# Kernel tuning notes

Hardware: AMD Instinct MI355X
Metric: run time of the kernel (lower is better)

## Reference

```python
import jax, jax.numpy as jnp
import numpy as np

D_MODEL = 1024
NUM_HEADS = 16
D_K = D_MODEL // NUM_HEADS
B, L = 2, 4096


def setup_inputs() -> dict:
    key = jax.random.key(0)
    ks = jax.random.split(key, 12)
    s = 0.02
    return {
        "q": jax.random.normal(ks[0], (B, L, D_MODEL), dtype=jnp.float32),
        "k": jax.random.normal(ks[1], (B, L, D_MODEL), dtype=jnp.float32),
        "v": jax.random.normal(ks[2], (B, L, D_MODEL), dtype=jnp.float32),
        "Wq": jax.random.normal(ks[3], (D_MODEL, D_MODEL), dtype=jnp.float32) * s,
        "bq": jax.random.normal(ks[4], (D_MODEL,), dtype=jnp.float32) * s,
        "Wk": jax.random.normal(ks[5], (D_MODEL, D_MODEL), dtype=jnp.float32) * s,
        "bk": jax.random.normal(ks[6], (D_MODEL,), dtype=jnp.float32) * s,
        "Wv": jax.random.normal(ks[7], (D_MODEL, D_MODEL), dtype=jnp.float32) * s,
        "bv": jax.random.normal(ks[8], (D_MODEL,), dtype=jnp.float32) * s,
        "Wo": jax.random.normal(ks[9], (D_MODEL, D_MODEL), dtype=jnp.float32) * s,
        "bo": jax.random.normal(ks[10], (D_MODEL,), dtype=jnp.float32) * s,
    }


def reference(q, k, v, Wq, bq, Wk, bk, Wv, bv, Wo, bo):
    b, l, _ = q.shape
    # projections (torch Linear: x @ W.T + b), reshape to [b, l, h, d]
    qf = (q @ Wq.T + bq).reshape(b, l, NUM_HEADS, D_K)
    kf = (k @ Wk.T + bk).reshape(b, l, NUM_HEADS, D_K)
    vf = (v @ Wv.T + bv).reshape(b, l, NUM_HEADS, D_K)
    # elu+1 feature map (positive features)
    qf = jax.nn.elu(qf) + 1.0
    kf = jax.nn.elu(kf) + 1.0
    # normalizer uses full-sequence k sum (as in the original code)
    z = 1.0 / (jnp.einsum("blhd,bhd->blh", qf, kf.sum(axis=1)) + 1e-6)
    # cumulative sums over sequence (the linear-attention scan state)
    k_cum = jnp.cumsum(kf, axis=1)  # [b, l, h, d]
    v_cum = jnp.cumsum(vf, axis=1)  # [b, l, h, d]
    context = jnp.einsum("blhd,blhd->blh", qf, k_cum)  # [b, l, h]
    context = context[..., None] * v_cum * z[..., None]  # [b, l, h, d]
    context = context.reshape(b, l, NUM_HEADS * D_K)
    return context @ Wo.T + bo
```

## Files before the change

kernel.cpp:

```cpp
#include <hip/hip_runtime.h>
#include <hip/hip_bf16.h>
#include <cstdint>
#include <cstddef>

#define D_MODEL 1024
#define NUM_HEADS 16
#define DK_DIM 64
#define BATCH 2
#define SEQ 4096
#define MROWS (BATCH*SEQ)
#define NCHUNK 128
#define CHUNK 32

#define BM 128
#define BN 128
#define BK 64
#define KTILES (D_MODEL/BK)

typedef __attribute__((ext_vector_type(4))) float f32x4;
typedef __attribute__((ext_vector_type(2))) float f32x2;
typedef __attribute__((ext_vector_type(8))) short bf16x8;
typedef __attribute__((ext_vector_type(4))) short s16x4;
typedef __attribute__((ext_vector_type(2))) uint32_t u32x2;
typedef __attribute__((ext_vector_type(4))) uint32_t u32x4;

__device__ __forceinline__ float b2f(short s) {
  union { uint32_t u; float f; } c; c.u = ((uint32_t)(uint16_t)s) << 16; return c.f;
}
__device__ __forceinline__ short f2b(float f) {
  union { float f; uint32_t u; } c; c.f = f;
  uint32_t u = c.u;
  u += 0x7FFFu + ((u >> 16) & 1u);
  return (short)(u >> 16);
}
__device__ __forceinline__ f32x4 b4_to_f4(s16x4 s) {
  f32x4 r;
  r.x = b2f(s.x); r.y = b2f(s.y); r.z = b2f(s.z); r.w = b2f(s.w);
  return r;
}
__device__ __forceinline__ uint32_t cvtpk(float lo, float hi) {
  uint32_t r;
  asm("v_cvt_pk_bf16_f32 %0, %1, %2" : "=v"(r) : "v"(lo), "v"(hi));
  return r;
}

__global__ __launch_bounds__(256) void cvt_w4(
    const float* __restrict__ s0, const float* __restrict__ s1,
    const float* __restrict__ s2, const float* __restrict__ s3,
    short* __restrict__ dst) {
  const int y = blockIdx.y;
  const float* s = (y == 0) ? s0 : (y == 1) ? s1 : (y == 2) ? s2 : s3;
  const int i = blockIdx.x * 256 + threadIdx.x;
  float4 v = reinterpret_cast<const float4*>(s)[i];
  s16x4 o;
  o.x = f2b(v.x); o.y = f2b(v.y); o.z = f2b(v.z); o.w = f2b(v.w);
  reinterpret_cast<s16x4*>(dst)[(size_t)y * (D_MODEL * D_MODEL / 4) + i] = o;
}

template<int AFP32, int OUTBF16>
__global__ __launch_bounds__(256, 3) void gemm4(
    const void* __restrict__ A0, const void* __restrict__ A1,
    const void* __restrict__ A2, const short* __restrict__ Wbase,
    const float* __restrict__ b0, const float* __restrict__ b1,
    const float* __restrict__ b2, void* __restrict__ Cbase, int actmask)
{
  __shared__ short lds[(BM + BN) * BK];
  const int tid = threadIdx.x;
  const int wid = tid >> 6;
  const int lane = tid & 63;
  const int brow = blockIdx.x * BM;
  const int bcol = blockIdx.y * BN;
  const int z = blockIdx.z;
  const int wr = wid >> 1, wc = wid & 1;

  const void* Ap = (z == 0) ? A0 : (z == 1) ? A1 : A2;
  const float* bias = (z == 0) ? b0 : (z == 1) ? b1 : b2;
  const short* Bw = Wbase + (size_t)z * D_MODEL * D_MODEL;
  const int act = (actmask >> z) & 1;
  const float* __restrict__ A32 = (const float*)Ap;
  const short* __restrict__ A16 = (const short*)Ap;

  f32x4 acc[4][4];
#pragma unroll
  for (int i = 0; i < 4; ++i)
#pragma unroll
    for (int j = 0; j < 4; ++j)
#pragma unroll
      for (int t = 0; t < 4; ++t) acc[i][j][t] = 0.f;

  const int srow = lane >> 3;
  const int gql  = lane & 7;

  float4 abuf32[8];
  u32x4  abuf16[4];

  auto loadA = [&](int t) {
    const int k0 = t * BK;
#pragma unroll
    for (int i = 0; i < 4; ++i) {
      const int row = brow + i * 32 + wid * 8 + srow;
      if constexpr (AFP32) {
        const float* src = A32 + (size_t)row * D_MODEL + k0 + gql * 8;
        abuf32[2 * i]     = *reinterpret_cast<const float4*>(src);
        abuf32[2 * i + 1] = *reinterpret_cast<const float4*>(src + 4);
      } else {
        abuf16[i] = *reinterpret_cast<const u32x4*>(A16 + (size_t)row * D_MODEL + k0 + gql * 8);
      }
    }
  };
  auto writeA = [&]() {
#pragma unroll
    for (int i = 0; i < 4; ++i) {
      u32x4 w;
      if constexpr (AFP32) {
        w.x = cvtpk(abuf32[2 * i].x,     abuf32[2 * i].y);
        w.y = cvtpk(abuf32[2 * i].z,     abuf32[2 * i].w);
        w.z = cvtpk(abuf32[2 * i + 1].x, abuf32[2 * i + 1].y);
        w.w = cvtpk(abuf32[2 * i + 1].z, abuf32[2 * i + 1].w);
      } else {
        w = abuf16[i];
      }
      const int ebyte = (i * 32 + wid * 8 + srow) * 128 + gql * 16;
      *reinterpret_cast<u32x4*>((char*)lds + ebyte) = w;
    }
  };
  auto stageB = [&](int t) {
    short* sB = lds + BM * BK;
    const int k0 = t * BK;
#pragma unroll
    for (int i = 0; i < 4; ++i) {
      const int r = i * 32 + wid * 8;
      const short* g = Bw + (size_t)(bcol + r + srow) * D_MODEL + k0 + gql * 8;
      __builtin_amdgcn_global_load_lds((const __attribute__((address_space(1))) void*)g,
          (__attribute__((address_space(3))) void*)(sB + r * BK), 16, 0, 0);
    }
  };

  const int lane15 = lane & 15;
  const int kq = (lane >> 4) * 16;

  auto compute = [&]() {
    const char* sAb = (const char*)lds;
    const char* sBb = sAb + BM * BK * 2;
#pragma unroll
    for (int ks = 0; ks < 2; ++ks) {
      bf16x8 Af[4], Bf[4];
#pragma unroll
      for (int mi = 0; mi < 4; ++mi)
        Af[mi] = *reinterpret_cast<const bf16x8*>(
            sAb + (wr * 64 + mi * 16 + lane15) * 128 + ks * 64 + kq);
#pragma unroll
      for (int nj = 0; nj < 4; ++nj)
        Bf[nj] = *reinterpret_cast<const bf16x8*>(
            sBb + (wc * 64 + nj * 16 + lane15) * 128 + ks * 64 + kq);
#pragma unroll
      for (int mi = 0; mi < 4; ++mi)
#pragma unroll
        for (int nj = 0; nj < 4; ++nj)
          acc[mi][nj] = __builtin_amdgcn_mfma_f32_16x16x32_bf16(Bf[nj], Af[mi], acc[mi][nj], 0, 0, 0);
    }
  };

  loadA(0);
#pragma unroll 1
  for (int t = 0; t < KTILES; ++t) {
    asm volatile("s_waitcnt lgkmcnt(0)" ::: "memory");
    __builtin_amdgcn_s_barrier();
    stageB(t);
    asm volatile("s_waitcnt vmcnt(4)" ::: "memory");
    writeA();
    if (t + 1 < KTILES) loadA(t + 1);
    asm volatile("s_waitcnt lgkmcnt(0)" ::: "memory");
    if (t + 1 < KTILES) {
      if constexpr (AFP32) asm volatile("s_waitcnt vmcnt(8)" ::: "memory");
      else                 asm volatile("s_waitcnt vmcnt(4)" ::: "memory");
    } else {
      asm volatile("s_waitcnt vmcnt(0)" ::: "memory");
    }
    __builtin_amdgcn_s_barrier();
    __builtin_amdgcn_sched_barrier(0);
    compute();
  }

  const int csub4 = (lane >> 4) * 4;
#pragma unroll
  for (int mi = 0; mi < 4; ++mi) {
    const int row = brow + wr * 64 + mi * 16 + lane15;
    const size_t rowbase = (size_t)z * MROWS * D_MODEL + (size_t)row * D_MODEL;
#pragma unroll
    for (int nj = 0; nj < 4; ++nj) {
      const int col0 = bcol + wc * 64 + nj * 16 + csub4;
      const float4 bv = *reinterpret_cast<const float4*>(&bias[col0]);
      float v0 = acc[mi][nj][0] + bv.x;
      float v1 = acc[mi][nj][1] + bv.y;
      float v2 = acc[mi][nj][2] + bv.z;
      float v3 = acc[mi][nj][3] + bv.w;
      if (act) {
        v0 = (v0 > 0.f) ? (v0 + 1.f) : __expf(v0);
        v1 = (v1 > 0.f) ? (v1 + 1.f) : __expf(v1);
        v2 = (v2 > 0.f) ? (v2 + 1.f) : __expf(v2);
        v3 = (v3 > 0.f) ? (v3 + 1.f) : __expf(v3);
      }
      if (OUTBF16) {
        u32x2 w;
        w.x = cvtpk(v0, v1);
        w.y = cvtpk(v2, v3);
        *reinterpret_cast<u32x2*>(&((short*)Cbase)[rowbase + col0]) = w;
      } else {
        float4 w; w.x = v0; w.y = v1; w.z = v2; w.w = v3;
        *reinterpret_cast<float4*>(&((float*)Cbase)[rowbase + col0]) = w;
      }
    }
  }
}

__global__ __launch_bounds__(256) void chunk_sums(
    const short* __restrict__ kf, const short* __restrict__ vf,
    float* __restrict__ ck, float* __restrict__ cv)
{
  const int gw = blockIdx.x * 4 + (threadIdx.x >> 6);
  const int lane = threadIdx.x & 63;
  const int c = gw & (NCHUNK - 1);
  const int h = (gw >> 7) & (NUM_HEADS - 1);
  const int b = gw >> 11;
  const int half = lane >> 5;
  const int dpair = (lane & 31) * 2;
  const size_t base = ((size_t)(b * SEQ + c * CHUNK) * NUM_HEADS + h) * DK_DIM + dpair;

  float skx = 0.f, sky = 0.f, svx = 0.f, svy = 0.f;
#pragma unroll
  for (int i = 0; i < CHUNK / 2; ++i) {
    const size_t off = base + (size_t)(2 * i + half) * D_MODEL;
    uint32_t ku = *reinterpret_cast<const uint32_t*>(&kf[off]);
    uint32_t vu = *reinterpret_cast<const uint32_t*>(&vf[off]);
    skx += b2f((short)(ku & 0xffff)); sky += b2f((short)(ku >> 16));
    svx += b2f((short)(vu & 0xffff)); svy += b2f((short)(vu >> 16));
  }
  skx += __shfl_xor(skx, 32, 64); sky += __shfl_xor(sky, 32, 64);
  svx += __shfl_xor(svx, 32, 64); svy += __shfl_xor(svy, 32, 64);
  if (half == 0) {
    const size_t o = ((size_t)((b * NUM_HEADS + h) * NCHUNK + c)) * DK_DIM + dpair;
    f32x2 a; a.x = skx; a.y = sky;
    f32x2 bb; bb.x = svx; bb.y = svy;
    *reinterpret_cast<f32x2*>(&ck[o]) = a;
    *reinterpret_cast<f32x2*>(&cv[o]) = bb;
  }
}

__global__ __launch_bounds__(64) void chunk_scan(
    float* __restrict__ ck, float* __restrict__ cv, float* __restrict__ ksum)
{
  const int bh = blockIdx.x;
  const int d = threadIdx.x;
  float rk = 0.f, rv = 0.f;
#pragma unroll 8
  for (int c = 0; c < NCHUNK; ++c) {
    const size_t o = ((size_t)(bh * NCHUNK + c)) * DK_DIM + d;
    const float tk = ck[o], tv = cv[o];
    ck[o] = rk; cv[o] = rv;
    rk += tk; rv += tv;
  }
  ksum[bh * DK_DIM + d] = rk;
}

__global__ __launch_bounds__(256) void scan_ctx(
    const short* __restrict__ qf, const short* __restrict__ kf,
    const short* __restrict__ vf,
    const float* __restrict__ ck, const float* __restrict__ cv,
    const float* __restrict__ ksum, short* __restrict__ ctx)
{
  const int gw = blockIdx.x * 4 + (threadIdx.x >> 6);
  const int lane = threadIdx.x & 63;
  const int pg = lane >> 4;
  const int dg = lane & 15;
  const int c = gw & (NCHUNK - 1);
  const int h = (gw >> 7) & (NUM_HEADS - 1);
  const int b = gw >> 11;
  const int bh = b * NUM_HEADS + h;
  const int d4 = dg * 4;

  f32x4 krun = *reinterpret_cast<const f32x4*>(
      &ck[((size_t)(bh * NCHUNK + c)) * DK_DIM + d4]);
  f32x4 vrun = *reinterpret_cast<const f32x4*>(
      &cv[((size_t)(bh * NCHUNK + c)) * DK_DIM + d4]);
  const f32x4 kst = *reinterpret_cast<const f32x4*>(&ksum[bh * DK_DIM + d4]);

  const size_t base = ((size_t)(b * SEQ + c * CHUNK) * NUM_HEADS + h) * DK_DIM + d4;

  for (int p0 = 0; p0 < CHUNK; p0 += 4) {
    const size_t qoff = base + (size_t)(p0 + pg) * D_MODEL;
    const f32x4 q4 = b4_to_f4(*reinterpret_cast<const s16x4*>(&qf[qoff]));
    f32x4 sk, sv;
#pragma unroll
    for (int i = 0; i < 4; ++i) {
      const size_t off = base + (size_t)(p0 + i) * D_MODEL;
      krun += b4_to_f4(*reinterpret_cast<const s16x4*>(&kf[off]));
      vrun += b4_to_f4(*reinterpret_cast<const s16x4*>(&vf[off]));
      if (i == pg) { sk = krun; sv = vrun; }
    }
    float s1 = q4.x * sk.x + q4.y * sk.y + q4.z * sk.z + q4.w * sk.w;
    float s2 = q4.x * kst.x + q4.y * kst.y + q4.z * kst.z + q4.w * kst.w;
#pragma unroll
    for (int m = 1; m < 16; m <<= 1) {
      s1 += __shfl_xor(s1, m, 64);
      s2 += __shfl_xor(s2, m, 64);
    }
    const float g = s1 / (s2 + 1e-6f);
    s16x4 o;
    o.x = f2b(g * sv.x); o.y = f2b(g * sv.y);
    o.z = f2b(g * sv.z); o.w = f2b(g * sv.w);
    *reinterpret_cast<s16x4*>(&ctx[qoff]) = o;
  }
}

extern "C" void kernel_launch(void* const* d_in, const int* in_sizes, int n_in,
                              void* d_out, int out_size, void* d_ws, size_t ws_size,
                              hipStream_t stream) {
  const float* q  = (const float*)d_in[0];
  const float* k  = (const float*)d_in[1];
  const float* v  = (const float*)d_in[2];
  const float* Wq = (const float*)d_in[3];
  const float* bq = (const float*)d_in[4];
  const float* Wk = (const float*)d_in[5];
  const float* bk = (const float*)d_in[6];
  const float* Wv = (const float*)d_in[7];
  const float* bv = (const float*)d_in[8];
  const float* Wo = (const float*)d_in[9];
  const float* bo = (const float*)d_in[10];
  float* out = (float*)d_out;

  uint8_t* p = (uint8_t*)d_ws;
  auto alloc = [&](size_t bytes) { uint8_t* r = p; p += bytes; return r; };
  short* qf  = (short*)alloc((size_t)MROWS * D_MODEL * 2);
  short* kf  = (short*)alloc((size_t)MROWS * D_MODEL * 2);
  short* vf  = (short*)alloc((size_t)MROWS * D_MODEL * 2);
  short* ctx = (short*)alloc((size_t)MROWS * D_MODEL * 2);
  short* Wqb = (short*)alloc((size_t)D_MODEL * D_MODEL * 2);
  short* Wkb = (short*)alloc((size_t)D_MODEL * D_MODEL * 2);
  short* Wvb = (short*)alloc((size_t)D_MODEL * D_MODEL * 2);
  short* Wob = (short*)alloc((size_t)D_MODEL * D_MODEL * 2);
  float* ck   = (float*)alloc((size_t)BATCH * NUM_HEADS * NCHUNK * DK_DIM * 4);
  float* cv   = (float*)alloc((size_t)BATCH * NUM_HEADS * NCHUNK * DK_DIM * 4);
  float* ksum = (float*)alloc((size_t)BATCH * NUM_HEADS * DK_DIM * 4);
  (void)Wkb; (void)Wvb;

  const dim3 gproj(MROWS / BM, D_MODEL / BN, 3);
  const dim3 gout (MROWS / BM, D_MODEL / BN, 1);

  cvt_w4<<<dim3(D_MODEL * D_MODEL / 4 / 256, 4), 256, 0, stream>>>(Wq, Wk, Wv, Wo, Wqb);

  gemm4<1, 1><<<gproj, 256, 0, stream>>>(q, k, v, Wqb, bq, bk, bv, qf, 0x3);

  chunk_sums<<<BATCH * NUM_HEADS * NCHUNK / 4, 256, 0, stream>>>(kf, vf, ck, cv);
  chunk_scan<<<BATCH * NUM_HEADS, 64, 0, stream>>>(ck, cv, ksum);
  scan_ctx<<<BATCH * NUM_HEADS * NCHUNK / 4, 256, 0, stream>>>(qf, kf, vf, ck, cv, ksum, ctx);

  gemm4<0, 0><<<gout, 256, 0, stream>>>(ctx, ctx, ctx, Wob, bo, bo, bo, out, 0);
}
```

Baseline: 150.5 us.

## Double-buffer GEMM LDS tiles and XOR-swizzle LDS layout

Turns the GEMM main loop into a two-slot LDS double buffer, so the next tile's B staging and A conversion/write happen while the current slot is computed, leaving one barrier per iteration instead of two. It also applies an XOR swizzle on the 16-byte column groups for both the A writes and the B global_load_lds source addresses, mirrored in the MFMA fragment reads, to cut LDS bank conflicts. The cost is twice the LDS (64 KB dynamic shared memory) and occupancy lowered to 2 blocks per CU in launch bounds.

New measurement: 145.4 us. -3.4%, faster.

```diff
diff --git a/kernel.cpp b/kernel.cpp
--- a/kernel.cpp
+++ b/kernel.cpp
@@ -15,6 +15,7 @@
 #define BM 128
 #define BN 128
 #define BK 64
+#define SLOT_SH ((BM+BN)*BK)
 #define KTILES (D_MODEL/BK)
 
 typedef __attribute__((ext_vector_type(4))) float f32x4;
@@ -58,13 +59,13 @@
 }
 
 template<int AFP32, int OUTBF16>
-__global__ __launch_bounds__(256, 3) void gemm4(
+__global__ __launch_bounds__(256, 2) void gemm4(
     const void* __restrict__ A0, const void* __restrict__ A1,
     const void* __restrict__ A2, const short* __restrict__ Wbase,
     const float* __restrict__ b0, const float* __restrict__ b1,
     const float* __restrict__ b2, void* __restrict__ Cbase, int actmask)
 {
-  __shared__ short lds[(BM + BN) * BK];
+  extern __shared__ __align__(16) short lds[];
   const int tid = threadIdx.x;
   const int wid = tid >> 6;
   const int lane = tid & 63;
@@ -90,6 +91,7 @@
 
   const int srow = lane >> 3;
   const int gql  = lane & 7;
+  const int sgel = (gql ^ srow) * 8;
 
   float4 abuf32[8];
   u32x4  abuf16[4];
@@ -108,7 +110,8 @@
       }
     }
   };
-  auto writeA = [&]() {
+  auto writeA = [&](int slot) {
+    char* sA = (char*)(lds + slot * SLOT_SH);
 #pragma unroll
     for (int i = 0; i < 4; ++i) {
       u32x4 w;
@@ -120,27 +123,28 @@
       } else {
         w = abuf16[i];
       }
-      const int ebyte = (i * 32 + wid * 8 + srow) * 128 + gql * 16;
-      *reinterpret_cast<u32x4*>((char*)lds + ebyte) = w;
+      const int ebyte = (i * 32 + wid * 8 + srow) * 128 + ((gql ^ srow) * 16);
+      *reinterpret_cast<u32x4*>(sA + ebyte) = w;
     }
   };
-  auto stageB = [&](int t) {
-    short* sB = lds + BM * BK;
+  auto stageB = [&](int t, int slot) {
+    short* sB = lds + slot * SLOT_SH + BM * BK;
     const int k0 = t * BK;
 #pragma unroll
     for (int i = 0; i < 4; ++i) {
       const int r = i * 32 + wid * 8;
-      const short* g = Bw + (size_t)(bcol + r + srow) * D_MODEL + k0 + gql * 8;
+      const short* g = Bw + (size_t)(bcol + r + srow) * D_MODEL + k0 + sgel;
       __builtin_amdgcn_global_load_lds((const __attribute__((address_space(1))) void*)g,
           (__attribute__((address_space(3))) void*)(sB + r * BK), 16, 0, 0);
     }
   };
 
   const int lane15 = lane & 15;
+  const int swz = (lane & 7) << 4;
   const int kq = (lane >> 4) * 16;
 
-  auto compute = [&]() {
-    const char* sAb = (const char*)lds;
+  auto compute = [&](int slot) {
+    const char* sAb = (const char*)(lds + slot * SLOT_SH);
     const char* sBb = sAb + BM * BK * 2;
 #pragma unroll
     for (int ks = 0; ks < 2; ++ks) {
@@ -148,11 +152,11 @@
 #pragma unroll
       for (int mi = 0; mi < 4; ++mi)
         Af[mi] = *reinterpret_cast<const bf16x8*>(
-            sAb + (wr * 64 + mi * 16 + lane15) * 128 + ks * 64 + kq);
+            sAb + (wr * 64 + mi * 16 + lane15) * 128 + ((ks * 64 + kq) ^ swz));
 #pragma unroll
       for (int nj = 0; nj < 4; ++nj)
         Bf[nj] = *reinterpret_cast<const bf16x8*>(
-            sBb + (wc * 64 + nj * 16 + lane15) * 128 + ks * 64 + kq);
+            sBb + (wc * 64 + nj * 16 + lane15) * 128 + ((ks * 64 + kq) ^ swz));
 #pragma unroll
       for (int mi = 0; mi < 4; ++mi)
 #pragma unroll
@@ -162,24 +166,27 @@
   };
 
   loadA(0);
+  asm volatile("s_waitcnt vmcnt(0)" ::: "memory");
+  writeA(0);
+  stageB(0, 0);
+  loadA(1);
+
 #pragma unroll 1
   for (int t = 0; t < KTILES; ++t) {
+    const int cur = t & 1;
     asm volatile("s_waitcnt lgkmcnt(0)" ::: "memory");
-    __builtin_amdgcn_s_barrier();
-    stageB(t);
-    asm volatile("s_waitcnt vmcnt(4)" ::: "memory");
-    writeA();
-    if (t + 1 < KTILES) loadA(t + 1);
-    asm volatile("s_waitcnt lgkmcnt(0)" ::: "memory");
-    if (t + 1 < KTILES) {
-      if constexpr (AFP32) asm volatile("s_waitcnt vmcnt(8)" ::: "memory");
-      else                 asm volatile("s_waitcnt vmcnt(4)" ::: "memory");
-    } else {
-      asm volatile("s_waitcnt vmcnt(0)" ::: "memory");
-    }
+    if (t == KTILES - 1) { asm volatile("s_waitcnt vmcnt(0)" ::: "memory"); }
+    else if constexpr (AFP32) { asm volatile("s_waitcnt vmcnt(8)" ::: "memory"); }
+    else                      { asm volatile("s_waitcnt vmcnt(4)" ::: "memory"); }
     __builtin_amdgcn_s_barrier();
     __builtin_amdgcn_sched_barrier(0);
-    compute();
+    if (t + 1 < KTILES) {
+      stageB(t + 1, cur ^ 1);
+      asm volatile("s_waitcnt vmcnt(4)" ::: "memory");
+      writeA(cur ^ 1);
+      if (t + 2 < KTILES) loadA(t + 2);
+    }
+    compute(cur);
   }
 
   const int csub4 = (lane >> 4) * 4;
@@ -346,14 +353,20 @@
 
   const dim3 gproj(MROWS / BM, D_MODEL / BN, 3);
   const dim3 gout (MROWS / BM, D_MODEL / BN, 1);
+  const int shbytes = 2 * SLOT_SH * (int)sizeof(short);
+
+  (void)hipFuncSetAttribute((const void*)gemm4<1, 1>,
+      hipFuncAttributeMaxDynamicSharedMemorySize, shbytes);
+  (void)hipFuncSetAttribute((const void*)gemm4<0, 0>,
+      hipFuncAttributeMaxDynamicSharedMemorySize, shbytes);
 
   cvt_w4<<<dim3(D_MODEL * D_MODEL / 4 / 256, 4), 256, 0, stream>>>(Wq, Wk, Wv, Wo, Wqb);
 
-  gemm4<1, 1><<<gproj, 256, 0, stream>>>(q, k, v, Wqb, bq, bk, bv, qf, 0x3);
+  gemm4<1, 1><<<gproj, 256, shbytes, stream>>>(q, k, v, Wqb, bq, bk, bv, qf, 0x3);
 
   chunk_sums<<<BATCH * NUM_HEADS * NCHUNK / 4, 256, 0, stream>>>(kf, vf, ck, cv);
   chunk_scan<<<BATCH * NUM_HEADS, 64, 0, stream>>>(ck, cv, ksum);
   scan_ctx<<<BATCH * NUM_HEADS * NCHUNK / 4, 256, 0, stream>>>(qf, kf, vf, ck, cv, ksum, ctx);
 
-  gemm4<0, 0><<<gout, 256, 0, stream>>>(ctx, ctx, ctx, Wob, bo, bo, bo, out, 0);
-}
+  gemm4<0, 0><<<gout, 256, shbytes, stream>>>(ctx, ctx, ctx, Wob, bo, bo, bo, out, 0);
+}
```
